# Kernel tuning notes

Hardware: AMD Instinct MI355X
Metric: run time of the kernel (lower is better)

The kernel has to match this reference:

```python
import math
import jax, jax.numpy as jnp
import numpy as np

B, S, DIM = 1, 1024, 2048
H, KVH, HD = 16, 4, 128
HID, L, VOCAB = 8192, 2, 32000
NIMG, TOK_START = 256, 1
IMG_IN = 2 * 14 * 14 * 3  # temporal_patch*spatial_patch^2*channels
EPS = 1e-6


def _rms(x, w=None, eps=EPS):
    y = x * jax.lax.rsqrt(jnp.mean(x * x, axis=-1, keepdims=True) + eps)
    return y if w is None else y * w


def _rope(x, angles):
    # x: [B,S,H,D], angles: [S, D//2] pairwise rotation angles (3D RoPE: 1D+2D concat)
    c = jnp.cos(angles)[None, :, None, :]
    s = jnp.sin(angles)[None, :, None, :]
    x1, x2 = x[..., 0::2], x[..., 1::2]
    return jnp.stack([x1 * c - x2 * s, x1 * s + x2 * c], axis=-1).reshape(x.shape)


def setup_inputs() -> dict:
    key = jax.random.key(0)
    ks = jax.random.split(key, 12)
    sc = 0.02
    return {
        "tokens": jax.random.randint(ks[0], (B, S), 0, VOCAB),
        "img_feats": jax.random.normal(ks[1], (B, NIMG, IMG_IN), jnp.float32),
        "freqs_cis": jax.random.normal(ks[2], (S, HD // 4), jnp.float32),
        "freqs_cis_2d": jax.random.normal(ks[3], (S, HD // 4), jnp.float32),
        "tok_emb": jax.random.normal(ks[4], (VOCAB, DIM), jnp.float32) * sc,
        "img_proj_w": jax.random.normal(ks[5], (DIM, IMG_IN), jnp.float32) * sc,
        "wqkv": jax.random.normal(ks[6], (L, H * HD + 2 * KVH * HD, DIM), jnp.float32) * sc,
        "wo": jax.random.normal(ks[7], (L, DIM, H * HD), jnp.float32) * sc,
        "sinks": jax.random.normal(ks[8], (L, H), jnp.float32),
        "w13": jax.random.normal(ks[9], (L, 2 * HID, DIM), jnp.float32) * sc,
        "w2": jax.random.normal(ks[10], (L, DIM, HID), jnp.float32) * sc,
        "norm_w": jnp.ones((DIM,), jnp.float32),
        "output_w": jax.random.normal(ks[11], (VOCAB, DIM), jnp.float32) * sc,
    }


def reference(tokens, img_feats, freqs_cis, freqs_cis_2d, tok_emb, img_proj_w,
              wqkv, wo, sinks, w13, w2, norm_w, output_w):
    # token embeddings + slice-based scatter of projected image tokens
    x = tok_emb[tokens]                                   # [B,S,DIM]
    img = jnp.einsum('bnf,df->bnd', img_feats, img_proj_w)
    x = jax.lax.dynamic_update_slice(x, img, (0, TOK_START, 0))

    angles = jnp.concatenate([freqs_cis, freqs_cis_2d], axis=-1)  # [S, HD//2]
    scale = 1.0 / math.sqrt(HD)
    neg = jnp.where(jnp.tril(jnp.ones((S, S), bool)), 0.0, -jnp.inf)  # causal
    n_rep = H // KVH
    q_dim, kv_dim = H * HD, KVH * HD

    for i in range(L):
        # attention: RMSNorm -> QKV -> QK-norm -> GQA expand -> RoPE -> SDPA+lse
        h = _rms(x)
        qkv = h @ wqkv[i].T
        q = qkv[..., :q_dim].reshape(B, S, H, HD)
        k = qkv[..., q_dim:q_dim + kv_dim].reshape(B, S, KVH, HD)
        v = qkv[..., q_dim + kv_dim:].reshape(B, S, KVH, HD)
        q, k = _rms(q), _rms(k)
        k = jnp.repeat(k, n_rep, axis=2)  # repeat_interleave over kv heads
        v = jnp.repeat(v, n_rep, axis=2)
        q, k = _rope(q, angles), _rope(k, angles)
        scores = jnp.einsum('bqhd,bkhd->bhqk', q, k) * scale + neg
        lse = jax.nn.logsumexp(scores, axis=-1)            # [B,H,S]
        attn = jnp.exp(scores - lse[..., None])
        out = jnp.einsum('bhqk,bkhd->bqhd', attn, v)        # [B,S,H,HD]
        sink_scale = jax.nn.sigmoid(lse - sinks[i][None, :, None])  # [B,H,S]
        out = out * sink_scale.transpose(0, 2, 1)[..., None]
        x = x + out.reshape(B, S, H * HD) @ wo[i].T

        # FFN: RMSNorm -> interleaved gate/up -> relu(gate)^2 * up -> down
        h = _rms(x)
        packed = h @ w13[i].T
        gate, up = packed[..., 0::2], packed[..., 1::2]
        x = x + (jnp.square(jax.nn.relu(gate)) * up) @ w2[i].T

    return _rms(x, norm_w) @ output_w.T                    # [B,S,VOCAB]
```

## Files before the change

### kernel.cpp

```cpp
#include <hip/hip_runtime.h>

typedef __bf16 bf16;
typedef bf16 bf16x8 __attribute__((ext_vector_type(8)));
typedef bf16 bf16x4 __attribute__((ext_vector_type(4)));
typedef bf16 bf16x2 __attribute__((ext_vector_type(2)));
typedef float f32x4 __attribute__((ext_vector_type(4)));
typedef float f32x2 __attribute__((ext_vector_type(2)));

#define S_LEN 1024
#define DIM 2048
#define NH 16
#define NKVH 4
#define HD 128
#define HID 8192
#define VOCAB 32000
#define QKV_N 3072
#define W13_N 16384
#define IMG_K 1176
#define NIMG 256

#define AS1 __attribute__((address_space(1)))
#define AS3 __attribute__((address_space(3)))

__device__ inline f32x4 mfma16(bf16x8 a, bf16x8 b, f32x4 c) {
  return __builtin_amdgcn_mfma_f32_16x16x32_bf16(a, b, c, 0, 0, 0);
}

__global__ void embed_kernel(const int* __restrict__ tok, const float* __restrict__ emb,
                             float* __restrict__ x) {
  int s = blockIdx.x, t = threadIdx.x;
  int id = tok[s];
  const float* er = emb + (size_t)id * DIM;
  float* xr = x + (size_t)s * DIM;
  *(f32x4*)(xr + t * 8)     = *(const f32x4*)(er + t * 8);
  *(f32x4*)(xr + t * 8 + 4) = *(const f32x4*)(er + t * 8 + 4);
}

__global__ void cvt_kernel(const float* __restrict__ in, bf16* __restrict__ o, int n) {
  int i = blockIdx.x * 256 + threadIdx.x;
  if (i < n) o[i] = (bf16)in[i];
}
__global__ void cvt4_kernel(const float* __restrict__ in, bf16* __restrict__ o, int n4) {
  int i = blockIdx.x * 256 + threadIdx.x;
  if (i < n4) {
    f32x4 v = *(const f32x4*)(in + (size_t)i * 4);
    bf16x4 b;
    b[0] = (bf16)v[0]; b[1] = (bf16)v[1]; b[2] = (bf16)v[2]; b[3] = (bf16)v[3];
    *(bf16x4*)(o + (size_t)i * 4) = b;
  }
}

template<int USE_W>
__global__ void rmsnorm_kernel(const float* __restrict__ x, const float* __restrict__ w,
                               bf16* __restrict__ o) {
  const int row = blockIdx.x, t = threadIdx.x;
  const float* xr = x + (size_t)row * DIM;
  f32x4 a = *(const f32x4*)(xr + t * 8);
  f32x4 b = *(const f32x4*)(xr + t * 8 + 4);
  float ss = a[0]*a[0] + a[1]*a[1] + a[2]*a[2] + a[3]*a[3]
           + b[0]*b[0] + b[1]*b[1] + b[2]*b[2] + b[3]*b[3];
#pragma unroll
  for (int off = 1; off < 64; off <<= 1) ss += __shfl_xor(ss, off);
  __shared__ float red[4];
  if ((t & 63) == 0) red[t >> 6] = ss;
  __syncthreads();
  ss = red[0] + red[1] + red[2] + red[3];
  float r = rsqrtf(ss * (1.0f / DIM) + 1e-6f);
  bf16x8 ov;
  if (USE_W) {
    f32x4 w1 = *(const f32x4*)(w + t * 8);
    f32x4 w2v = *(const f32x4*)(w + t * 8 + 4);
    ov[0] = (bf16)(a[0]*r*w1[0]); ov[1] = (bf16)(a[1]*r*w1[1]);
    ov[2] = (bf16)(a[2]*r*w1[2]); ov[3] = (bf16)(a[3]*r*w1[3]);
    ov[4] = (bf16)(b[0]*r*w2v[0]); ov[5] = (bf16)(b[1]*r*w2v[1]);
    ov[6] = (bf16)(b[2]*r*w2v[2]); ov[7] = (bf16)(b[3]*r*w2v[3]);
  } else {
    ov[0] = (bf16)(a[0]*r); ov[1] = (bf16)(a[1]*r);
    ov[2] = (bf16)(a[2]*r); ov[3] = (bf16)(a[3]*r);
    ov[4] = (bf16)(b[0]*r); ov[5] = (bf16)(b[1]*r);
    ov[6] = (bf16)(b[2]*r); ov[7] = (bf16)(b[3]*r);
  }
  *(bf16x8*)(o + (size_t)row * DIM + t * 8) = ov;
}

__global__ void qkvpost_kernel(const float* __restrict__ qkv, const float* __restrict__ f1,
                               const float* __restrict__ f2, bf16* __restrict__ qb,
                               bf16* __restrict__ kb, bf16* __restrict__ vtb) {
  int s = blockIdx.x, t = threadIdx.x;
  __shared__ float cs[64], sn[64];
  if (t < 64) {
    float ang = (t < 32) ? f1[(size_t)s * 32 + t] : f2[(size_t)s * 32 + (t - 32)];
    cs[t] = cosf(ang);
    sn[t] = sinf(ang);
  }
  __syncthreads();
  int w = t >> 6, lane = t & 63;
  for (int hh = w; hh < 24; hh += 4) {
    const float* base = qkv + (size_t)s * QKV_N + hh * HD;
    f32x2 e = *(const f32x2*)(base + lane * 2);
    if (hh < 20) {
      float ssum = e[0]*e[0] + e[1]*e[1];
#pragma unroll
      for (int off = 1; off < 64; off <<= 1) ssum += __shfl_xor(ssum, off);
      float r = rsqrtf(ssum * (1.0f / HD) + 1e-6f);
      float x1 = e[0] * r, x2 = e[1] * r;
      float c = cs[lane], s2 = sn[lane];
      bf16x2 ov;
      ov[0] = (bf16)(x1 * c - x2 * s2);
      ov[1] = (bf16)(x1 * s2 + x2 * c);
      if (hh < 16)
        *(bf16x2*)(qb + ((size_t)hh * S_LEN + s) * HD + lane * 2) = ov;
      else
        *(bf16x2*)(kb + ((size_t)(hh - 16) * S_LEN + s) * HD + lane * 2) = ov;
    } else {
      int kv = hh - 20;
      vtb[((size_t)kv * HD + lane * 2) * S_LEN + s]     = (bf16)e[0];
      vtb[((size_t)kv * HD + lane * 2 + 1) * S_LEN + s] = (bf16)e[1];
    }
  }
}

__global__ __launch_bounds__(256) void attn_kernel(const bf16* __restrict__ qb,
                                                   const bf16* __restrict__ kb,
                                                   const bf16* __restrict__ vtb,
                                                   const float* __restrict__ sinks,
                                                   bf16* __restrict__ out) {
  const int h = blockIdx.y, qs = blockIdx.x;
  const int w = threadIdx.x >> 6, lane = threadIdx.x & 63;
  const int lo = lane & 15, hi = lane >> 4;
  const int q0 = qs * 16;
  const int q = q0 + lo;
  const int kvh = h >> 2;
  const bf16* Q = qb + (size_t)h * S_LEN * HD;
  const bf16* Kp = kb + (size_t)kvh * S_LEN * HD;
  const bf16* Vt = vtb + (size_t)kvh * HD * S_LEN;
  const float scale = 0.08838834764831845f;

  __shared__ float accS[4][64 * 36];
  __shared__ float mS[4][16], lS[4][16];

  bf16x8 qf[4];
#pragma unroll
  for (int ks = 0; ks < 4; ++ks)
    qf[ks] = *(const bf16x8*)(Q + (size_t)q * HD + ks * 32 + hi * 8);

  f32x4 accT[8];
#pragma unroll
  for (int i = 0; i < 8; ++i) accT[i] = (f32x4){0.f, 0.f, 0.f, 0.f};
  float mrow = -3e38f, lrow = 0.f;

  const int nt = (q0 + 15) / 32 + 1;
  for (int tile = w; tile < nt; tile += 4) {
    const int kv0 = tile * 32;
    f32x4 st0 = (f32x4){0.f,0.f,0.f,0.f}, st1 = (f32x4){0.f,0.f,0.f,0.f};
#pragma unroll
    for (int ks = 0; ks < 4; ++ks) {
      const bf16* kbase = Kp + (size_t)(kv0 + lo) * HD + ks * 32 + hi * 8;
      bf16x8 k0f = *(const bf16x8*)(kbase);
      bf16x8 k1f = *(const bf16x8*)(kbase + 16 * HD);
      st0 = mfma16(k0f, qf[ks], st0);
      st1 = mfma16(k1f, qf[ks], st1);
    }
    float p[2][4];
    float pmax = -3e38f;
#pragma unroll
    for (int r = 0; r < 4; ++r) {
      int kvg0 = kv0 + hi * 4 + r;
      float v0 = (kvg0 <= q) ? st0[r] * scale : -3e38f;
      int kvg1 = kvg0 + 16;
      float v1 = (kvg1 <= q) ? st1[r] * scale : -3e38f;
      p[0][r] = v0; p[1][r] = v1;
      pmax = fmaxf(pmax, fmaxf(v0, v1));
    }
    pmax = fmaxf(pmax, __shfl_xor(pmax, 16));
    pmax = fmaxf(pmax, __shfl_xor(pmax, 32));
    float mnew = fmaxf(mrow, pmax);
    float alpha = __expf(mrow - mnew);
    float ps = 0.f;
#pragma unroll
    for (int f = 0; f < 2; ++f)
#pragma unroll
      for (int r = 0; r < 4; ++r) {
        float e = __expf(p[f][r] - mnew);
        p[f][r] = e;
        ps += e;
      }
    ps += __shfl_xor(ps, 16);
    ps += __shfl_xor(ps, 32);
    lrow = lrow * alpha + ps;
    mrow = mnew;
#pragma unroll
    for (int fd = 0; fd < 8; ++fd) {
      accT[fd][0] *= alpha; accT[fd][1] *= alpha;
      accT[fd][2] *= alpha; accT[fd][3] *= alpha;
    }
    bf16x8 pb;
#pragma unroll
    for (int j = 0; j < 8; ++j) {
      int src = ((j >> 2) + 2 * (hi & 1)) * 16 + lo;
      float v0 = __shfl(p[0][j & 3], src);
      float v1 = __shfl(p[1][j & 3], src);
      pb[j] = (bf16)((hi >= 2) ? v1 : v0);
    }
#pragma unroll
    for (int fd = 0; fd < 8; ++fd) {
      bf16x8 vf = *(const bf16x8*)(Vt + (size_t)(fd * 16 + lo) * S_LEN + kv0 + hi * 8);
      accT[fd] = mfma16(vf, pb, accT[fd]);
    }
  }
  if (hi == 0) { mS[w][lo] = mrow; lS[w][lo] = lrow; }
  float* as = &accS[w][lane * 36];
#pragma unroll
  for (int fd = 0; fd < 8; ++fd) *(f32x4*)(as + fd * 4) = accT[fd];
  __syncthreads();
  float m0 = mS[0][lo], m1 = mS[1][lo], m2 = mS[2][lo], m3 = mS[3][lo];
  float mstar = fmaxf(fmaxf(m0, m1), fmaxf(m2, m3));
  float e0 = __expf(m0 - mstar), e1 = __expf(m1 - mstar);
  float e2 = __expf(m2 - mstar), e3 = __expf(m3 - mstar);
  float lstar = lS[0][lo]*e0 + lS[1][lo]*e1 + lS[2][lo]*e2 + lS[3][lo]*e3;
  float lse = mstar + __logf(lstar);
  float ssig = 1.f / (1.f + __expf(sinks[h] - lse));
  float sc = ssig / lstar;
#pragma unroll
  for (int f2 = 0; f2 < 2; ++f2) {
    int fd = w * 2 + f2;
    f32x4 a0 = *(const f32x4*)&accS[0][lane * 36 + fd * 4];
    f32x4 a1 = *(const f32x4*)&accS[1][lane * 36 + fd * 4];
    f32x4 a2 = *(const f32x4*)&accS[2][lane * 36 + fd * 4];
    f32x4 a3 = *(const f32x4*)&accS[3][lane * 36 + fd * 4];
#pragma unroll
    for (int r = 0; r < 4; ++r) {
      float o = a0[r]*e0 + a1[r]*e1 + a2[r]*e2 + a3[r]*e3;
      out[(size_t)q * DIM + h * HD + fd * 16 + hi * 4 + r] = (bf16)(o * sc);
    }
  }
}

__device__ inline void xcd_remap(int ntm, int ntn, int& mtile, int& ntile) {
  const int flat = blockIdx.x + ntm * blockIdx.y;
  const int chunk = ntm * 8;
  const int gfull = ntn >> 3;
  const int g = flat / chunk;
  if (g < gfull) {
    int rem = flat - g * chunk;
    ntile = g * 8 + (rem & 7);
    mtile = rem >> 3;
  } else {
    int rem = flat - gfull * chunk;
    int nrem = ntn - gfull * 8;
    ntile = gfull * 8 + rem % nrem;
    mtile = rem / nrem;
  }
}

enum { EPI_STORE = 0, EPI_ADD = 1, EPI_ACT = 2 };

template<int BM, int BN, int EPI, int GL>
__global__ void gemm_bt(const bf16* __restrict__ A, const float* __restrict__ W,
                        float* __restrict__ C, bf16* __restrict__ Cb,
                        int M, int N, int K, int ldc) {
  constexpr int BK = 64;
  __shared__ __align__(16) char lds[(BM + BN) * BK * 2];
  char* ldsA = lds;
  char* ldsB = lds + BM * BK * 2;
  const int t = threadIdx.x;
  int mtile, ntile;
  xcd_remap(gridDim.x, gridDim.y, mtile, ntile);
  const int m0 = mtile * BM, n0 = ntile * BN;

  const int wid = t >> 6, lane = t & 63;
  const int lo = lane & 15, hi = lane >> 4;
  const int wr = wid >> 1, wc = wid & 1;
  constexpr int TM = BM / 32, TN = BN / 32;
  constexpr int NA = BM / 32;
  constexpr int NPASS = BM / 32;
  constexpr int NW = BN / 16;

  f32x4 acc[TM][TN];
#pragma unroll
  for (int m = 0; m < TM; ++m)
#pragma unroll
    for (int n = 0; n < TN; ++n) acc[m][n] = (f32x4){0.f, 0.f, 0.f, 0.f};

  const int nk = (K + BK - 1) / BK;
  for (int kt = 0; kt < nk; ++kt) {
    const int k0 = kt * BK;
    bf16x8 av[NA];
    f32x4 wv[NW];
    if (!GL) {
#pragma unroll
      for (int i = 0; i < NA; ++i) {
        int c = t + i * 256;
        int row = c >> 3, kc = c & 7;
        int kg = k0 + kc * 8;
        bf16x8 z = {};
        av[i] = (kg < K) ? *(const bf16x8*)(A + (size_t)(m0 + row) * K + kg) : z;
      }
    }
#pragma unroll
    for (int i = 0; i < NW; ++i) {
      int c = t + i * 256;
      int row = c >> 4, kc = c & 15;
      int kg = k0 + kc * 4;
      f32x4 z = (f32x4){0.f, 0.f, 0.f, 0.f};
      wv[i] = (kg < K) ? *(const f32x4*)(W + (size_t)(n0 + row) * K + kg) : z;
    }
    __syncthreads();
    if (GL) {
#pragma unroll
      for (int i = 0; i < NPASS; ++i) {
        int row = i * 32 + (t >> 3);
        int srcb = ((t & 7) * 16) ^ ((row & 7) << 4);
        const bf16* g2 = A + (size_t)(m0 + row) * K + k0 + (srcb >> 1);
        char* l = ldsA + i * 4096 + wid * 1024;
        __builtin_amdgcn_global_load_lds((const AS1 void*)g2, (AS3 void*)l, 16, 0, 0);
      }
    } else {
#pragma unroll
      for (int i = 0; i < NA; ++i) {
        int c = t + i * 256;
        int row = c >> 3, kc = c & 7;
        int kb = (kc * 16) ^ ((row & 7) << 4);
        *(bf16x8*)(ldsA + row * 128 + kb) = av[i];
      }
    }
#pragma unroll
    for (int i = 0; i < NW; ++i) {
      int c = t + i * 256;
      int row = c >> 4, kc = c & 15;
      bf16x4 bv;
      bv[0] = (bf16)wv[i][0]; bv[1] = (bf16)wv[i][1];
      bv[2] = (bf16)wv[i][2]; bv[3] = (bf16)wv[i][3];
      int kb = (kc * 8) ^ ((row & 7) << 4);
      *(bf16x4*)(ldsB + row * 128 + kb) = bv;
    }
    __syncthreads();
#pragma unroll
    for (int ks = 0; ks < 2; ++ks) {
      bf16x8 af[TM], bfr[TN];
      int kbb = ks * 64 + hi * 16;
#pragma unroll
      for (int m = 0; m < TM; ++m) {
        int row = wr * (BM / 2) + m * 16 + lo;
        af[m] = *(const bf16x8*)(ldsA + row * 128 + (kbb ^ ((row & 7) << 4)));
      }
#pragma unroll
      for (int n = 0; n < TN; ++n) {
        int row = wc * (BN / 2) + n * 16 + lo;
        bfr[n] = *(const bf16x8*)(ldsB + row * 128 + (kbb ^ ((row & 7) << 4)));
      }
#pragma unroll
      for (int m = 0; m < TM; ++m)
#pragma unroll
        for (int n = 0; n < TN; ++n)
          acc[m][n] = mfma16(af[m], bfr[n], acc[m][n]);
    }
    __syncthreads();
  }
#pragma unroll
  for (int m = 0; m < TM; ++m) {
    int gmb = m0 + wr * (BM / 2) + m * 16 + hi * 4;
#pragma unroll
    for (int n = 0; n < TN; ++n) {
      int gn = n0 + wc * (BN / 2) + n * 16 + lo;
#pragma unroll
      for (int r = 0; r < 4; ++r) {
        float v = acc[m][n][r];
        if (EPI == EPI_STORE) {
          C[(size_t)(gmb + r) * ldc + gn] = v;
        } else if (EPI == EPI_ADD) {
          C[(size_t)(gmb + r) * ldc + gn] += v;
        } else {
          float pv = __shfl_xor(v, 1);
          if (!(lane & 1)) {
            float g2 = fmaxf(v, 0.f);
            Cb[(size_t)(gmb + r) * (W13_N / 2) + (gn >> 1)] = (bf16)(g2 * g2 * pv);
          }
        }
      }
    }
  }
}

template<int BM, int BN, int EPI>
__global__ __launch_bounds__(256) void gemm_bb(const bf16* __restrict__ A,
                                               const bf16* __restrict__ W,
                                               float* __restrict__ C, bf16* __restrict__ Cb,
                                               int K, int ldc) {
  constexpr int BK = 64;
  __shared__ __align__(16) char lds[(BM + BN) * BK * 2];
  char* ldsA = lds;
  char* ldsB = lds + BM * BK * 2;
  const int t = threadIdx.x;
  int mtile, ntile;
  xcd_remap(gridDim.x, gridDim.y, mtile, ntile);
  const int m0 = mtile * BM, n0 = ntile * BN;

  const int wid = t >> 6, lane = t & 63;
  const int lo = lane & 15, hi = lane >> 4;
  const int wr = wid >> 1, wc = wid & 1;
  constexpr int TM = BM / 32, TN = BN / 32;
  constexpr int PA = BM / 32, PB = BN / 32;

  f32x4 acc[TM][TN];
#pragma unroll
  for (int m = 0; m < TM; ++m)
#pragma unroll
    for (int n = 0; n < TN; ++n) acc[m][n] = (f32x4){0.f, 0.f, 0.f, 0.f};

  const int prow = t >> 3;
  const int psrcb = (t & 7) * 16;
  const int nk = K / BK;
  for (int kt = 0; kt < nk; ++kt) {
    const int k0 = kt * BK;
#pragma unroll
    for (int i = 0; i < PA; ++i) {
      int row = i * 32 + prow;
      int srcb = psrcb ^ ((row & 7) << 4);
      const bf16* g = A + (size_t)(m0 + row) * K + k0 + (srcb >> 1);
      __builtin_amdgcn_global_load_lds((const AS1 void*)g,
                                       (AS3 void*)(ldsA + i * 4096 + wid * 1024), 16, 0, 0);
    }
#pragma unroll
    for (int i = 0; i < PB; ++i) {
      int row = i * 32 + prow;
      int srcb = psrcb ^ ((row & 7) << 4);
      const bf16* g = W + (size_t)(n0 + row) * K + k0 + (srcb >> 1);
      __builtin_amdgcn_global_load_lds((const AS1 void*)g,
                                       (AS3 void*)(ldsB + i * 4096 + wid * 1024), 16, 0, 0);
    }
    __syncthreads();
#pragma unroll
    for (int ks = 0; ks < 2; ++ks) {
      bf16x8 af[TM], bfr[TN];
      int kbb = ks * 64 + hi * 16;
#pragma unroll
      for (int m = 0; m < TM; ++m) {
        int row = wr * (BM / 2) + m * 16 + lo;
        af[m] = *(const bf16x8*)(ldsA + row * 128 + (kbb ^ ((row & 7) << 4)));
      }
#pragma unroll
      for (int n = 0; n < TN; ++n) {
        int row = wc * (BN / 2) + n * 16 + lo;
        bfr[n] = *(const bf16x8*)(ldsB + row * 128 + (kbb ^ ((row & 7) << 4)));
      }
#pragma unroll
      for (int m = 0; m < TM; ++m)
#pragma unroll
        for (int n = 0; n < TN; ++n)
          acc[m][n] = mfma16(af[m], bfr[n], acc[m][n]);
    }
    __syncthreads();
  }
#pragma unroll
  for (int m = 0; m < TM; ++m) {
    int gmb = m0 + wr * (BM / 2) + m * 16 + hi * 4;
#pragma unroll
    for (int n = 0; n < TN; ++n) {
      int gn = n0 + wc * (BN / 2) + n * 16 + lo;
#pragma unroll
      for (int r = 0; r < 4; ++r) {
        float v = acc[m][n][r];
        if (EPI == EPI_STORE) {
          C[(size_t)(gmb + r) * ldc + gn] = v;
        } else if (EPI == EPI_ADD) {
          C[(size_t)(gmb + r) * ldc + gn] += v;
        } else {
          float pv = __shfl_xor(v, 1);
          if (!(lane & 1)) {
            float g2 = fmaxf(v, 0.f);
            Cb[(size_t)(gmb + r) * (W13_N / 2) + (gn >> 1)] = (bf16)(g2 * g2 * pv);
          }
        }
      }
    }
  }
}

template<int EPI>
__global__ __launch_bounds__(512, 1) void gemm_2pf(const bf16* __restrict__ A,
                                                   const float* __restrict__ W,
                                                   float* __restrict__ C, bf16* __restrict__ Cb,
                                                   int K, int ldc) {
  extern __shared__ __align__(16) char lds[];
  char* ldsA = lds;
  char* ldsB = lds + 65536;
  const int t = threadIdx.x;
  int mtile, ntile;
  xcd_remap(gridDim.x, gridDim.y, mtile, ntile);
  const int m0 = mtile * 256, n0 = ntile * 256;
  const int wid = t >> 6, lane = t & 63;
  const int lo = lane & 15, hi = lane >> 4;
  const int wr = wid >> 2, wc = wid & 3;

  f32x4 acc[8][4];
#pragma unroll
  for (int f = 0; f < 8; ++f)
#pragma unroll
    for (int g = 0; g < 4; ++g) acc[f][g] = (f32x4){0.f, 0.f, 0.f, 0.f};

  const int prow = t >> 3;
  const int pcol = (t & 7) * 16;

  auto STAGEA = [&](int h, int kt2) {
    char* dst = ldsA + (kt2 & 1) * 32768 + h * 16384;
    const int k0 = kt2 * 64;
#pragma unroll
    for (int i = 0; i < 2; ++i) {
      int row = i * 64 + prow;
      int srcb = pcol ^ ((row & 7) << 4);
      const bf16* g = A + (size_t)(m0 + h * 128 + row) * K + k0 + (srcb >> 1);
      __builtin_amdgcn_global_load_lds((const AS1 void*)g,
          (AS3 void*)(dst + i * 8192 + wid * 1024), 16, 0, 0);
    }
  };

  f32x4 breg[4][2];
  auto BLOAD = [&](int kt2) {
#pragma unroll
    for (int i = 0; i < 4; ++i) {
      int c = t + i * 512;
      int row = c >> 3, kc = c & 7;
      const float* g = W + (size_t)(n0 + row) * K + kt2 * 64 + kc * 8;
      breg[i][0] = *(const f32x4*)(g);
      breg[i][1] = *(const f32x4*)(g + 4);
    }
  };
  auto BWRITE = [&](int kt2) {
#pragma unroll
    for (int i = 0; i < 4; ++i) {
      int c = t + i * 512;
      int row = c >> 3, kc = c & 7;
      int h = row >> 7, rowh = row & 127;
      bf16x8 bv;
#pragma unroll
      for (int e = 0; e < 4; ++e) {
        bv[e]     = (bf16)breg[i][0][e];
        bv[4 + e] = (bf16)breg[i][1][e];
      }
      *(bf16x8*)(ldsB + (kt2 & 1) * 32768 + h * 16384 + rowh * 128 +
                 ((kc * 16) ^ ((rowh & 7) << 4))) = bv;
    }
  };

  auto LDA = [&](int buf, int mh, int i, int ks) -> bf16x8 {
    int row = (mh * 4 + i) * 16 + lo;
    return *(const bf16x8*)(ldsA + buf * 32768 + wr * 16384 + row * 128 +
                            ((ks * 64 + hi * 16) ^ ((row & 7) << 4)));
  };
  auto LDB = [&](int buf, int nh, int j, int ks) -> bf16x8 {
    int rowh = (wc & 1) * 64 + (nh * 2 + j) * 16 + lo;
    return *(const bf16x8*)(ldsB + buf * 32768 + (wc >> 1) * 16384 + rowh * 128 +
                            ((ks * 64 + hi * 16) ^ ((rowh & 7) << 4)));
  };

  const int nk = K / 64;
  BLOAD(0);
  STAGEA(0, 0);
  STAGEA(1, 0);
  BWRITE(0);
  asm volatile("s_waitcnt vmcnt(0) lgkmcnt(0)" ::: "memory");
  __builtin_amdgcn_s_barrier();

  for (int kt = 0; kt < nk; ++kt) {
    const int buf = kt & 1;
    const bool more = (kt + 1) < nk;
    if (more) {
      BLOAD(kt + 1);
      STAGEA(0, kt + 1);
      STAGEA(1, kt + 1);
    }
#pragma unroll
    for (int mh = 0; mh < 2; ++mh) {
      bf16x8 a[4][2];
#pragma unroll
      for (int i = 0; i < 4; ++i) { a[i][0] = LDA(buf, mh, i, 0); a[i][1] = LDA(buf, mh, i, 1); }
#pragma unroll
      for (int nh = 0; nh < 2; ++nh) {
        bf16x8 b[2][2];
#pragma unroll
        for (int j = 0; j < 2; ++j) { b[j][0] = LDB(buf, nh, j, 0); b[j][1] = LDB(buf, nh, j, 1); }
        asm volatile("s_waitcnt lgkmcnt(0)" ::: "memory");
        __builtin_amdgcn_sched_barrier(0);
        __builtin_amdgcn_s_setprio(1);
#pragma unroll
        for (int i = 0; i < 4; ++i)
#pragma unroll
          for (int j = 0; j < 2; ++j) {
            acc[mh * 4 + i][nh * 2 + j] = mfma16(a[i][0], b[j][0], acc[mh * 4 + i][nh * 2 + j]);
            acc[mh * 4 + i][nh * 2 + j] = mfma16(a[i][1], b[j][1], acc[mh * 4 + i][nh * 2 + j]);
          }
        __builtin_amdgcn_s_setprio(0);
      }
    }
    if (more) BWRITE(kt + 1);
    asm volatile("s_waitcnt vmcnt(0) lgkmcnt(0)" ::: "memory");
    __builtin_amdgcn_s_barrier();
  }
#pragma unroll
  for (int f = 0; f < 8; ++f) {
    int gmb = m0 + wr * 128 + f * 16 + hi * 4;
#pragma unroll
    for (int g = 0; g < 4; ++g) {
      int gn = n0 + wc * 64 + g * 16 + lo;
#pragma unroll
      for (int r = 0; r < 4; ++r) {
        float v = acc[f][g][r];
        if (EPI == EPI_STORE) {
          C[(size_t)(gmb + r) * ldc + gn] = v;
        } else if (EPI == EPI_ADD) {
          C[(size_t)(gmb + r) * ldc + gn] += v;
        } else {
          float pv = __shfl_xor(v, 1);
          if (!(lane & 1)) {
            float g2 = fmaxf(v, 0.f);
            Cb[(size_t)(gmb + r) * (W13_N / 2) + (gn >> 1)] = (bf16)(g2 * g2 * pv);
          }
        }
      }
    }
  }
}

extern "C" void kernel_launch(void* const* d_in, const int* in_sizes, int n_in,
                              void* d_out, int out_size, void* d_ws, size_t ws_size,
                              hipStream_t stream) {
  const int* tokens = (const int*)d_in[0];
  const float* img_feats = (const float*)d_in[1];
  const float* freqs = (const float*)d_in[2];
  const float* freqs2 = (const float*)d_in[3];
  const float* tok_emb = (const float*)d_in[4];
  const float* img_proj_w = (const float*)d_in[5];
  const float* wqkv = (const float*)d_in[6];
  const float* wo = (const float*)d_in[7];
  const float* sinks = (const float*)d_in[8];
  const float* w13 = (const float*)d_in[9];
  const float* w2 = (const float*)d_in[10];
  const float* norm_w = (const float*)d_in[11];
  const float* output_w = (const float*)d_in[12];
  float* out = (float*)d_out;

  char* ws = (char*)d_ws;
  float* x = (float*)ws;   ws += (size_t)S_LEN * DIM * 4;
  bf16* h = (bf16*)ws;     ws += (size_t)S_LEN * DIM * 2;
  float* qkv = (float*)ws; ws += (size_t)S_LEN * QKV_N * 4;
  bf16* qb = (bf16*)ws;    ws += (size_t)NH * S_LEN * HD * 2;
  bf16* kb = (bf16*)ws;    ws += (size_t)NKVH * S_LEN * HD * 2;
  bf16* vtb = (bf16*)ws;   ws += (size_t)NKVH * HD * S_LEN * 2;
  bf16* ao = (bf16*)ws;    ws += (size_t)S_LEN * DIM * 2;
  bf16* act = (bf16*)ws;   ws += (size_t)S_LEN * HID * 2;
  bf16* imgb = (bf16*)ws;  ws += (size_t)NIMG * IMG_K * 2;
  const size_t n_wqkv = (size_t)2 * QKV_N * DIM;
  const size_t n_wo   = (size_t)2 * DIM * (NH * HD);
  const size_t n_w2   = (size_t)2 * DIM * HID;
  bf16* wqkvb = (bf16*)ws; ws += n_wqkv * 2;
  bf16* wob   = (bf16*)ws; ws += n_wo * 2;
  bf16* w2b   = (bf16*)ws; ws += n_w2 * 2;
  const bool bf16_path = ((size_t)(ws - (char*)d_ws) <= ws_size);

  bool big_ok = false;
  {
    hipError_t e1 = hipFuncSetAttribute((const void*)&gemm_2pf<EPI_STORE>,
                                        hipFuncAttributeMaxDynamicSharedMemorySize, 131072);
    hipError_t e2 = hipFuncSetAttribute((const void*)&gemm_2pf<EPI_ACT>,
                                        hipFuncAttributeMaxDynamicSharedMemorySize, 131072);
    if (e1 == hipSuccess && e2 == hipSuccess) {
      hipFuncAttributes fa1{}, fa2{};
      if (hipFuncGetAttributes(&fa1, (const void*)&gemm_2pf<EPI_STORE>) == hipSuccess &&
          hipFuncGetAttributes(&fa2, (const void*)&gemm_2pf<EPI_ACT>) == hipSuccess)
        big_ok = fa1.maxDynamicSharedSizeBytes >= 131072 &&
                 fa2.maxDynamicSharedSizeBytes >= 131072;
    }
  }

  embed_kernel<<<S_LEN, 256, 0, stream>>>(tokens, tok_emb, x);
  cvt_kernel<<<(NIMG * IMG_K + 255) / 256, 256, 0, stream>>>(img_feats, imgb, NIMG * IMG_K);
  gemm_bt<64, 128, EPI_STORE, 0><<<dim3(NIMG / 64, DIM / 128), 256, 0, stream>>>(
      imgb, img_proj_w, x + DIM, nullptr, NIMG, DIM, IMG_K, DIM);

  if (bf16_path) {
    cvt4_kernel<<<(int)(n_wqkv / 4 + 255) / 256, 256, 0, stream>>>(wqkv, wqkvb, (int)(n_wqkv / 4));
    cvt4_kernel<<<(int)(n_wo / 4 + 255) / 256, 256, 0, stream>>>(wo, wob, (int)(n_wo / 4));
    cvt4_kernel<<<(int)(n_w2 / 4 + 255) / 256, 256, 0, stream>>>(w2, w2b, (int)(n_w2 / 4));
  }

  for (int i = 0; i < 2; ++i) {
    rmsnorm_kernel<0><<<S_LEN, 256, 0, stream>>>(x, nullptr, h);
    if (bf16_path) {
      gemm_bb<64, 128, EPI_STORE><<<dim3(S_LEN / 64, QKV_N / 128), 256, 0, stream>>>(
          h, wqkvb + (size_t)i * QKV_N * DIM, qkv, nullptr, DIM, QKV_N);
    } else {
      gemm_bt<64, 128, EPI_STORE, 1><<<dim3(S_LEN / 64, QKV_N / 128), 256, 0, stream>>>(
          h, wqkv + (size_t)i * QKV_N * DIM, qkv, nullptr, S_LEN, QKV_N, DIM, QKV_N);
    }
    qkvpost_kernel<<<S_LEN, 256, 0, stream>>>(qkv, freqs, freqs2, qb, kb, vtb);
    attn_kernel<<<dim3(S_LEN / 16, NH), 256, 0, stream>>>(qb, kb, vtb, sinks + i * NH, ao);
    if (bf16_path) {
      gemm_bb<64, 128, EPI_ADD><<<dim3(S_LEN / 64, DIM / 128), 256, 0, stream>>>(
          ao, wob + (size_t)i * DIM * DIM, x, nullptr, DIM, DIM);
    } else {
      gemm_bt<64, 128, EPI_ADD, 1><<<dim3(S_LEN / 64, DIM / 128), 256, 0, stream>>>(
          ao, wo + (size_t)i * DIM * DIM, x, nullptr, S_LEN, DIM, DIM, DIM);
    }
    rmsnorm_kernel<0><<<S_LEN, 256, 0, stream>>>(x, nullptr, h);
    if (big_ok) {
      gemm_2pf<EPI_ACT><<<dim3(S_LEN / 256, W13_N / 256), 512, 131072, stream>>>(
          h, w13 + (size_t)i * W13_N * DIM, nullptr, act, DIM, 0);
    } else {
      gemm_bt<128, 128, EPI_ACT, 1><<<dim3(S_LEN / 128, W13_N / 128), 256, 0, stream>>>(
          h, w13 + (size_t)i * W13_N * DIM, nullptr, act, S_LEN, W13_N, DIM, 0);
    }
    if (bf16_path) {
      gemm_bb<64, 128, EPI_ADD><<<dim3(S_LEN / 64, DIM / 128), 256, 0, stream>>>(
          act, w2b + (size_t)i * DIM * HID, x, nullptr, HID, DIM);
    } else {
      gemm_bt<64, 128, EPI_ADD, 1><<<dim3(S_LEN / 64, DIM / 128), 256, 0, stream>>>(
          act, w2 + (size_t)i * DIM * HID, x, nullptr, S_LEN, DIM, HID, DIM);
    }
  }
  rmsnorm_kernel<1><<<S_LEN, 256, 0, stream>>>(x, norm_w, h);
  if (big_ok) {
    gemm_2pf<EPI_STORE><<<dim3(S_LEN / 256, VOCAB / 256), 512, 131072, stream>>>(
        h, output_w, out, nullptr, DIM, VOCAB);
  } else {
    gemm_bt<128, 128, EPI_STORE, 1><<<dim3(S_LEN / 128, VOCAB / 128), 256, 0, stream>>>(
        h, output_w, out, nullptr, S_LEN, VOCAB, DIM, VOCAB);
  }
}
```

Measured before the change: 1.049 ms.

## Restructure big GEMM into four-phase ping-pong schedule with split B staging

Rewrites the 256x256 GEMM main loop into four quadrant phases, each with its own LDS fragment loads, barrier and MFMA block. The fp32 B-tile loads and bf16 conversion writes are split into two halves and interleaved across the phases instead of one bulk load and write per k-step. Warp-to-tile mapping changes so each wave computes strided 64x32 sub-blocks in every quadrant, with the epilogue indexing updated to match. The aim is better overlap of global loads, LDS traffic and MFMA work, in exchange for more barriers per iteration and more register pressure.

New measurement: 1.066 ms. No clear change (+1.6%).

```diff
diff --git a/kernel.cpp b/kernel.cpp
--- a/kernel.cpp
+++ b/kernel.cpp
@@ -478,10 +478,10 @@
 }
 
 template<int EPI>
-__global__ __launch_bounds__(512, 1) void gemm_2pf(const bf16* __restrict__ A,
-                                                   const float* __restrict__ W,
-                                                   float* __restrict__ C, bf16* __restrict__ Cb,
-                                                   int K, int ldc) {
+__global__ __launch_bounds__(512, 1) void gemm_4p(const bf16* __restrict__ A,
+                                                  const float* __restrict__ W,
+                                                  float* __restrict__ C, bf16* __restrict__ Cb,
+                                                  int K, int ldc) {
   extern __shared__ __align__(16) char lds[];
   char* ldsA = lds;
   char* ldsB = lds + 65536;
@@ -515,94 +515,137 @@
     }
   };
 
-  f32x4 breg[4][2];
-  auto BLOAD = [&](int kt2) {
-#pragma unroll
-    for (int i = 0; i < 4; ++i) {
+  f32x4 breg0[2][2], breg1[2][2];
+  auto BLOADH = [&](f32x4 (&br)[2][2], int h, int kt2) {
+#pragma unroll
+    for (int i = 0; i < 2; ++i) {
       int c = t + i * 512;
       int row = c >> 3, kc = c & 7;
-      const float* g = W + (size_t)(n0 + row) * K + kt2 * 64 + kc * 8;
-      breg[i][0] = *(const f32x4*)(g);
-      breg[i][1] = *(const f32x4*)(g + 4);
+      const float* g = W + (size_t)(n0 + h * 128 + row) * K + kt2 * 64 + kc * 8;
+      br[i][0] = *(const f32x4*)(g);
+      br[i][1] = *(const f32x4*)(g + 4);
     }
   };
-  auto BWRITE = [&](int kt2) {
-#pragma unroll
-    for (int i = 0; i < 4; ++i) {
+  auto BWRITEH = [&](f32x4 (&br)[2][2], int h, int kt2) {
+#pragma unroll
+    for (int i = 0; i < 2; ++i) {
       int c = t + i * 512;
       int row = c >> 3, kc = c & 7;
-      int h = row >> 7, rowh = row & 127;
       bf16x8 bv;
 #pragma unroll
       for (int e = 0; e < 4; ++e) {
-        bv[e]     = (bf16)breg[i][0][e];
-        bv[4 + e] = (bf16)breg[i][1][e];
-      }
-      *(bf16x8*)(ldsB + (kt2 & 1) * 32768 + h * 16384 + rowh * 128 +
-                 ((kc * 16) ^ ((rowh & 7) << 4))) = bv;
+        bv[e]     = (bf16)br[i][0][e];
+        bv[4 + e] = (bf16)br[i][1][e];
+      }
+      *(bf16x8*)(ldsB + (kt2 & 1) * 32768 + h * 16384 + row * 128 +
+                 ((kc * 16) ^ ((row & 7) << 4))) = bv;
     }
   };
 
   auto LDA = [&](int buf, int mh, int i, int ks) -> bf16x8 {
-    int row = (mh * 4 + i) * 16 + lo;
-    return *(const bf16x8*)(ldsA + buf * 32768 + wr * 16384 + row * 128 +
+    int row = wr * 64 + i * 16 + lo;
+    return *(const bf16x8*)(ldsA + buf * 32768 + mh * 16384 + row * 128 +
                             ((ks * 64 + hi * 16) ^ ((row & 7) << 4)));
   };
   auto LDB = [&](int buf, int nh, int j, int ks) -> bf16x8 {
-    int rowh = (wc & 1) * 64 + (nh * 2 + j) * 16 + lo;
-    return *(const bf16x8*)(ldsB + buf * 32768 + (wc >> 1) * 16384 + rowh * 128 +
-                            ((ks * 64 + hi * 16) ^ ((rowh & 7) << 4)));
+    int row = wc * 32 + j * 16 + lo;
+    return *(const bf16x8*)(ldsB + buf * 32768 + nh * 16384 + row * 128 +
+                            ((ks * 64 + hi * 16) ^ ((row & 7) << 4)));
   };
 
   const int nk = K / 64;
-  BLOAD(0);
+  bf16x8 a[4][2], b[2][2];
+
   STAGEA(0, 0);
   STAGEA(1, 0);
-  BWRITE(0);
-  asm volatile("s_waitcnt vmcnt(0) lgkmcnt(0)" ::: "memory");
+  __builtin_amdgcn_sched_barrier(0);
+  BLOADH(breg0, 0, 0);
+  BWRITEH(breg0, 0, 0);
+  __builtin_amdgcn_sched_barrier(0);
+  BLOADH(breg1, 1, 0);
+  asm volatile("s_waitcnt lgkmcnt(0)" ::: "memory");
   __builtin_amdgcn_s_barrier();
 
   for (int kt = 0; kt < nk; ++kt) {
     const int buf = kt & 1;
     const bool more = (kt + 1) < nk;
+    BWRITEH(breg1, 1, kt);
+#pragma unroll
+    for (int i = 0; i < 4; ++i) { a[i][0] = LDA(buf, 0, i, 0); a[i][1] = LDA(buf, 0, i, 1); }
+#pragma unroll
+    for (int j = 0; j < 2; ++j) { b[j][0] = LDB(buf, 0, j, 0); b[j][1] = LDB(buf, 0, j, 1); }
     if (more) {
-      BLOAD(kt + 1);
       STAGEA(0, kt + 1);
+      __builtin_amdgcn_sched_barrier(0);
+      BLOADH(breg0, 0, kt + 1);
+    }
+    asm volatile("s_waitcnt lgkmcnt(0)" ::: "memory");
+    __builtin_amdgcn_sched_barrier(0);
+    __builtin_amdgcn_s_setprio(1);
+#pragma unroll
+    for (int i = 0; i < 4; ++i)
+#pragma unroll
+      for (int j = 0; j < 2; ++j) {
+        acc[i][j] = mfma16(a[i][0], b[j][0], acc[i][j]);
+        acc[i][j] = mfma16(a[i][1], b[j][1], acc[i][j]);
+      }
+    __builtin_amdgcn_s_setprio(0);
+    __builtin_amdgcn_s_barrier();
+#pragma unroll
+    for (int j = 0; j < 2; ++j) { b[j][0] = LDB(buf, 1, j, 0); b[j][1] = LDB(buf, 1, j, 1); }
+    asm volatile("s_waitcnt lgkmcnt(0)" ::: "memory");
+    __builtin_amdgcn_sched_barrier(0);
+    __builtin_amdgcn_s_setprio(1);
+#pragma unroll
+    for (int i = 0; i < 4; ++i)
+#pragma unroll
+      for (int j = 0; j < 2; ++j) {
+        acc[i][2 + j] = mfma16(a[i][0], b[j][0], acc[i][2 + j]);
+        acc[i][2 + j] = mfma16(a[i][1], b[j][1], acc[i][2 + j]);
+      }
+    __builtin_amdgcn_s_setprio(0);
+    __builtin_amdgcn_s_barrier();
+#pragma unroll
+    for (int i = 0; i < 4; ++i) { a[i][0] = LDA(buf, 1, i, 0); a[i][1] = LDA(buf, 1, i, 1); }
+    if (more) {
       STAGEA(1, kt + 1);
-    }
-#pragma unroll
-    for (int mh = 0; mh < 2; ++mh) {
-      bf16x8 a[4][2];
-#pragma unroll
-      for (int i = 0; i < 4; ++i) { a[i][0] = LDA(buf, mh, i, 0); a[i][1] = LDA(buf, mh, i, 1); }
-#pragma unroll
-      for (int nh = 0; nh < 2; ++nh) {
-        bf16x8 b[2][2];
-#pragma unroll
-        for (int j = 0; j < 2; ++j) { b[j][0] = LDB(buf, nh, j, 0); b[j][1] = LDB(buf, nh, j, 1); }
-        asm volatile("s_waitcnt lgkmcnt(0)" ::: "memory");
-        __builtin_amdgcn_sched_barrier(0);
-        __builtin_amdgcn_s_setprio(1);
-#pragma unroll
-        for (int i = 0; i < 4; ++i)
-#pragma unroll
-          for (int j = 0; j < 2; ++j) {
-            acc[mh * 4 + i][nh * 2 + j] = mfma16(a[i][0], b[j][0], acc[mh * 4 + i][nh * 2 + j]);
-            acc[mh * 4 + i][nh * 2 + j] = mfma16(a[i][1], b[j][1], acc[mh * 4 + i][nh * 2 + j]);
-          }
-        __builtin_amdgcn_s_setprio(0);
-      }
-    }
-    if (more) BWRITE(kt + 1);
-    asm volatile("s_waitcnt vmcnt(0) lgkmcnt(0)" ::: "memory");
+      __builtin_amdgcn_sched_barrier(0);
+      BLOADH(breg1, 1, kt + 1);
+    }
+    asm volatile("s_waitcnt lgkmcnt(0)" ::: "memory");
+    __builtin_amdgcn_sched_barrier(0);
+    __builtin_amdgcn_s_setprio(1);
+#pragma unroll
+    for (int i = 0; i < 4; ++i)
+#pragma unroll
+      for (int j = 0; j < 2; ++j) {
+        acc[4 + i][2 + j] = mfma16(a[i][0], b[j][0], acc[4 + i][2 + j]);
+        acc[4 + i][2 + j] = mfma16(a[i][1], b[j][1], acc[4 + i][2 + j]);
+      }
+    __builtin_amdgcn_s_setprio(0);
     __builtin_amdgcn_s_barrier();
+#pragma unroll
+    for (int j = 0; j < 2; ++j) { b[j][0] = LDB(buf, 0, j, 0); b[j][1] = LDB(buf, 0, j, 1); }
+    if (more) BWRITEH(breg0, 0, kt + 1);
+    asm volatile("s_waitcnt lgkmcnt(0)" ::: "memory");
+    __builtin_amdgcn_sched_barrier(0);
+    __builtin_amdgcn_s_setprio(1);
+#pragma unroll
+    for (int i = 0; i < 4; ++i)
+#pragma unroll
+      for (int j = 0; j < 2; ++j) {
+        acc[4 + i][j] = mfma16(a[i][0], b[j][0], acc[4 + i][j]);
+        acc[4 + i][j] = mfma16(a[i][1], b[j][1], acc[4 + i][j]);
+      }
+    __builtin_amdgcn_s_setprio(0);
+    __builtin_amdgcn_s_barrier();
   }
 #pragma unroll
   for (int f = 0; f < 8; ++f) {
-    int gmb = m0 + wr * 128 + f * 16 + hi * 4;
+    int gmb = m0 + (f >> 2) * 128 + wr * 64 + (f & 3) * 16 + hi * 4;
 #pragma unroll
     for (int g = 0; g < 4; ++g) {
-      int gn = n0 + wc * 64 + g * 16 + lo;
+      int gn = n0 + (g >> 1) * 128 + wc * 32 + (g & 1) * 16 + lo;
 #pragma unroll
       for (int r = 0; r < 4; ++r) {
         float v = acc[f][g][r];
@@ -660,14 +703,14 @@
 
   bool big_ok = false;
   {
-    hipError_t e1 = hipFuncSetAttribute((const void*)&gemm_2pf<EPI_STORE>,
+    hipError_t e1 = hipFuncSetAttribute((const void*)&gemm_4p<EPI_STORE>,
                                         hipFuncAttributeMaxDynamicSharedMemorySize, 131072);
-    hipError_t e2 = hipFuncSetAttribute((const void*)&gemm_2pf<EPI_ACT>,
+    hipError_t e2 = hipFuncSetAttribute((const void*)&gemm_4p<EPI_ACT>,
                                         hipFuncAttributeMaxDynamicSharedMemorySize, 131072);
     if (e1 == hipSuccess && e2 == hipSuccess) {
       hipFuncAttributes fa1{}, fa2{};
-      if (hipFuncGetAttributes(&fa1, (const void*)&gemm_2pf<EPI_STORE>) == hipSuccess &&
-          hipFuncGetAttributes(&fa2, (const void*)&gemm_2pf<EPI_ACT>) == hipSuccess)
+      if (hipFuncGetAttributes(&fa1, (const void*)&gemm_4p<EPI_STORE>) == hipSuccess &&
+          hipFuncGetAttributes(&fa2, (const void*)&gemm_4p<EPI_ACT>) == hipSuccess)
         big_ok = fa1.maxDynamicSharedSizeBytes >= 131072 &&
                  fa2.maxDynamicSharedSizeBytes >= 131072;
     }
@@ -704,7 +747,7 @@
     }
     rmsnorm_kernel<0><<<S_LEN, 256, 0, stream>>>(x, nullptr, h);
     if (big_ok) {
-      gemm_2pf<EPI_ACT><<<dim3(S_LEN / 256, W13_N / 256), 512, 131072, stream>>>(
+      gemm_4p<EPI_ACT><<<dim3(S_LEN / 256, W13_N / 256), 512, 131072, stream>>>(
           h, w13 + (size_t)i * W13_N * DIM, nullptr, act, DIM, 0);
     } else {
       gemm_bt<128, 128, EPI_ACT, 1><<<dim3(S_LEN / 128, W13_N / 128), 256, 0, stream>>>(
@@ -720,7 +763,7 @@
   }
   rmsnorm_kernel<1><<<S_LEN, 256, 0, stream>>>(x, norm_w, h);
   if (big_ok) {
-    gemm_2pf<EPI_STORE><<<dim3(S_LEN / 256, VOCAB / 256), 512, 131072, stream>>>(
+    gemm_4p<EPI_STORE><<<dim3(S_LEN / 256, VOCAB / 256), 512, 131072, stream>>>(
         h, output_w, out, nullptr, DIM, VOCAB);
   } else {
     gemm_bt<128, 128, EPI_STORE, 1><<<dim3(S_LEN / 128, VOCAB / 128), 256, 0, stream>>>(
```
